# Kernel optimization log

Hardware: AMD Instinct MI355X
Metric: run time of the kernel (lower is better)

The kernel has to match this reference:

```python
import math
import jax, jax.numpy as jnp
import numpy as np

N_EXPERTS = 8
CAPACITY_FACTOR = 1.25
AUX_COEF = 0.01  # forward passes aux_loss_coef to BOTH z-loss and lb-loss


def setup_inputs() -> dict:
    key = jax.random.key(0)
    k1, k2 = jax.random.split(key)
    B, T, D = 4, 4096, 2048
    x = jax.random.normal(k1, (B, T, D), dtype=jnp.float32)
    # nn.Linear(d_model, n_experts, bias=False) weight: (n_experts, d_model)
    W = jax.random.normal(k2, (N_EXPERTS, D), dtype=jnp.float32) * (1.0 / math.sqrt(D))
    return {"x": x, "W": W}


def reference(x, W):
    B, T, D = x.shape
    S = B * T
    E = W.shape[0]
    capacity = int(math.ceil(S / E * CAPACITY_FACTOR))  # static

    x_flat = x.reshape(S, D)
    logits = jnp.einsum("sd,ed->se", x_flat, W)          # (S, E)
    probs = jax.nn.softmax(logits, axis=-1)               # (S, E)
    gate_vals = jnp.max(probs, axis=-1)                   # (S,)
    expert_idx = jnp.argmax(probs, axis=-1)               # (S,) int

    # rank of each token within its expert's queue (token order), 0-based
    onehot = jax.nn.one_hot(expert_idx, E, dtype=jnp.int32)        # (S, E)
    rank = jnp.sum(jnp.cumsum(onehot, axis=0) * onehot, axis=-1) - 1  # (S,)
    keep = rank < capacity
    kept_gates = jnp.where(keep, gate_vals, jnp.zeros((), gate_vals.dtype))

    # z-loss: coef * mean(logsumexp(logits)^2)
    log_z = jax.scipy.special.logsumexp(logits, axis=-1)
    z_loss = AUX_COEF * jnp.mean(log_z * log_z)

    # load-balance loss: coef * E * sum(f_i * p_i)
    p = jnp.mean(probs, axis=0)                                     # (E,)
    counts = jnp.zeros((E,), dtype=probs.dtype).at[expert_idx].add(1.0)
    f = counts / S
    lb_loss = AUX_COEF * E * jnp.sum(f * p)

    aux_loss = z_loss + lb_loss
    return expert_idx, kept_gates, aux_loss
```

## Files before the change

### kernel.cpp

```cpp
#include <hip/hip_runtime.h>

#define S_TOKENS 16384
#define DMODEL   2048
#define NE       8
#define CAPACITY 2560
#define AUXC     0.01f


__global__ void init_kernel(float* __restrict__ acc) {
    int t = threadIdx.x;
    if (t < 9) acc[t] = 0.0f;
}

__global__ __launch_bounds__(512, 1) void logits_kernel(
    const float* __restrict__ x, const float* __restrict__ W,
    int* __restrict__ idx_out, float* __restrict__ gate_out,
    float* __restrict__ psum, float* __restrict__ zsum) {
    __shared__ float4 WA[DMODEL];
    __shared__ float4 WB[DMODEL];

    const int tid  = threadIdx.x;
    const int wave = tid >> 6;
    const int lane = tid & 63;

    for (int j = tid; j < DMODEL; j += 512) {
        WA[j] = make_float4(W[j],          W[DMODEL + j],   W[2*DMODEL + j], W[3*DMODEL + j]);
        WB[j] = make_float4(W[4*DMODEL+j], W[5*DMODEL + j], W[6*DMODEL + j], W[7*DMODEL + j]);
    }
    __syncthreads();

    float pacc = 0.0f;
    float zacc = 0.0f;

    for (int gi = 0; gi < 4; ++gi) {
        const int group = blockIdx.x * 4 + gi;
        const int token = group * 8 + wave;
        const float* __restrict__ xrow = x + (size_t)token * DMODEL;

        float a0=0,a1=0,a2=0,a3=0,a4=0,a5=0,a6=0,a7=0;
        #pragma unroll 8
        for (int k = 0; k < DMODEL/64; ++k) {
            float  xv = xrow[k*64 + lane];
            float4 wa = WA[k*64 + lane];
            float4 wb = WB[k*64 + lane];
            a0 += xv*wa.x; a1 += xv*wa.y; a2 += xv*wa.z; a3 += xv*wa.w;
            a4 += xv*wb.x; a5 += xv*wb.y; a6 += xv*wb.z; a7 += xv*wb.w;
        }
        #pragma unroll
        for (int off = 32; off > 0; off >>= 1) {
            a0 += __shfl_xor(a0, off); a1 += __shfl_xor(a1, off);
            a2 += __shfl_xor(a2, off); a3 += __shfl_xor(a3, off);
            a4 += __shfl_xor(a4, off); a5 += __shfl_xor(a5, off);
            a6 += __shfl_xor(a6, off); a7 += __shfl_xor(a7, off);
        }
        float m = a0; int e = 0;
        if (a1 > m) { m = a1; e = 1; }
        if (a2 > m) { m = a2; e = 2; }
        if (a3 > m) { m = a3; e = 3; }
        if (a4 > m) { m = a4; e = 4; }
        if (a5 > m) { m = a5; e = 5; }
        if (a6 > m) { m = a6; e = 6; }
        if (a7 > m) { m = a7; e = 7; }
        float z = expf(a0-m)+expf(a1-m)+expf(a2-m)+expf(a3-m)
                + expf(a4-m)+expf(a5-m)+expf(a6-m)+expf(a7-m);
        float gate = 1.0f / z;
        float lz   = m + logf(z);

        if (lane == 0) {
            idx_out[token]  = e;
            gate_out[token] = gate;
            zacc += lz * lz;
        }
        float ae = a0;
        if (lane == 1) ae = a1;
        if (lane == 2) ae = a2;
        if (lane == 3) ae = a3;
        if (lane == 4) ae = a4;
        if (lane == 5) ae = a5;
        if (lane == 6) ae = a6;
        if (lane == 7) ae = a7;
        if (lane < NE) pacc += expf(ae - m) * gate;
    }

    __syncthreads();
    float* red = (float*)WA;
    float* zrd = (float*)WB;
    if (lane < NE)  red[wave*8 + lane] = pacc;
    if (lane == 0)  zrd[wave] = zacc;
    __syncthreads();
    if (tid < NE) {
        float s = 0.0f;
        #pragma unroll
        for (int w = 0; w < 8; ++w) s += red[w*8 + tid];
        atomicAdd(&psum[tid], s);
    }
    if (tid == NE) {
        float s = 0.0f;
        #pragma unroll
        for (int w = 0; w < 8; ++w) s += zrd[w];
        atomicAdd(zsum, s);
    }
}

__global__ __launch_bounds__(256, 1) void scan_kernel(
    const int* __restrict__ idx, int* __restrict__ prefix,
    const float* __restrict__ psum, const float* __restrict__ zsum,
    float* __restrict__ aux_out) {
    __shared__ int arr[NE][256];
    const int t = threadIdx.x;

    unsigned clo = 0, chi = 0;
    const int base = t * 64;
    #pragma unroll 8
    for (int i = 0; i < 64; ++i) {
        int e = idx[base + i];
        if (e < 4) clo += 1u << (8*e);
        else       chi += 1u << (8*(e-4));
    }
    int cnt[8];
    cnt[0] = clo & 255; cnt[1] = (clo >> 8) & 255; cnt[2] = (clo >> 16) & 255; cnt[3] = clo >> 24;
    cnt[4] = chi & 255; cnt[5] = (chi >> 8) & 255; cnt[6] = (chi >> 16) & 255; cnt[7] = chi >> 24;
    #pragma unroll
    for (int e = 0; e < NE; ++e) arr[e][t] = cnt[e];
    __syncthreads();

    for (int off = 1; off < 256; off <<= 1) {
        int v[8];
        #pragma unroll
        for (int e = 0; e < NE; ++e) v[e] = (t >= off) ? arr[e][t - off] : 0;
        __syncthreads();
        #pragma unroll
        for (int e = 0; e < NE; ++e) arr[e][t] += v[e];
        __syncthreads();
    }
    #pragma unroll
    for (int e = 0; e < NE; ++e) prefix[t*8 + e] = arr[e][t] - cnt[e];

    if (t == 0) {
        float lb = 0.0f;
        for (int e = 0; e < NE; ++e) {
            float f = (float)arr[e][255] / (float)S_TOKENS;
            float p = psum[e] / (float)S_TOKENS;
            lb += f * p;
        }
        lb *= AUXC * (float)NE;
        float zl = AUXC * (zsum[0] / (float)S_TOKENS);
        aux_out[0] = zl + lb;
    }
}

__global__ __launch_bounds__(64, 1) void output_kernel(
    const int* __restrict__ idx, const float* __restrict__ gate,
    const int* __restrict__ prefix, float* __restrict__ out) {
    const int b = blockIdx.x;
    const int l = threadIdx.x;
    const int token = b*64 + l;
    const int e = idx[token];

    unsigned long long mymask = 0;
    #pragma unroll
    for (int q = 0; q < NE; ++q) {
        unsigned long long msk = __ballot(e == q);
        if (e == q) mymask = msk;
    }
    unsigned long long lt = (1ull << l) - 1ull;
    int rank = prefix[b*8 + e] + __popcll(mymask & lt);

    out[token] = (float)e;
    out[S_TOKENS + token] = (rank < CAPACITY) ? gate[token] : 0.0f;
}

extern "C" void kernel_launch(void* const* d_in, const int* in_sizes, int n_in,
                              void* d_out, int out_size, void* d_ws, size_t ws_size,
                              hipStream_t stream) {
    const float* x = (const float*)d_in[0];
    const float* W = (const float*)d_in[1];
    float* out = (float*)d_out;

    int*   ws_idx    = (int*)d_ws;
    float* ws_gate   = (float*)d_ws + 16384;
    int*   ws_prefix = (int*)d_ws + 32768;
    float* ws_psum   = (float*)d_ws + 34816;
    float* ws_zsum   = (float*)d_ws + 34824;

    init_kernel<<<1, 64, 0, stream>>>(ws_psum);
    logits_kernel<<<512, 512, 0, stream>>>(x, W, ws_idx, ws_gate, ws_psum, ws_zsum);
    scan_kernel<<<1, 256, 0, stream>>>(ws_idx, ws_prefix, ws_psum, ws_zsum, out + 2*S_TOKENS);
    output_kernel<<<256, 64, 0, stream>>>(ws_idx, ws_gate, ws_prefix, out);
}
```

Measured before the change: 209.7 us.

## Register-block 4 tokens per wave with float4 loads and drop atomics/init kernel

```diff
diff --git a/kernel.cpp b/kernel.cpp
--- a/kernel.cpp
+++ b/kernel.cpp
@@ -7,115 +7,149 @@
 #define AUXC     0.01f
 
 
-__global__ void init_kernel(float* __restrict__ acc) {
-    int t = threadIdx.x;
-    if (t < 9) acc[t] = 0.0f;
-}
-
-__global__ __launch_bounds__(512, 1) void logits_kernel(
+__global__ __launch_bounds__(512, 4) void logits_kernel(
     const float* __restrict__ x, const float* __restrict__ W,
     int* __restrict__ idx_out, float* __restrict__ gate_out,
-    float* __restrict__ psum, float* __restrict__ zsum) {
-    __shared__ float4 WA[DMODEL];
-    __shared__ float4 WB[DMODEL];
+    float* __restrict__ bsums) {
+    __shared__ float4 WE[NE * 512];
 
     const int tid  = threadIdx.x;
     const int wave = tid >> 6;
     const int lane = tid & 63;
 
-    for (int j = tid; j < DMODEL; j += 512) {
-        WA[j] = make_float4(W[j],          W[DMODEL + j],   W[2*DMODEL + j], W[3*DMODEL + j]);
-        WB[j] = make_float4(W[4*DMODEL+j], W[5*DMODEL + j], W[6*DMODEL + j], W[7*DMODEL + j]);
-    }
-    __syncthreads();
+    {
+        const float4* __restrict__ Wf4 = (const float4*)W;
+        #pragma unroll
+        for (int i = 0; i < 8; ++i) WE[i * 512 + tid] = Wf4[i * 512 + tid];
+    }
+    __syncthreads();
+
+    const int t0 = blockIdx.x * 32 + wave * 4;
+    const float4* __restrict__ xr0 = (const float4*)x + (size_t)(t0 + 0) * (DMODEL / 4);
+    const float4* __restrict__ xr1 = (const float4*)x + (size_t)(t0 + 1) * (DMODEL / 4);
+    const float4* __restrict__ xr2 = (const float4*)x + (size_t)(t0 + 2) * (DMODEL / 4);
+    const float4* __restrict__ xr3 = (const float4*)x + (size_t)(t0 + 3) * (DMODEL / 4);
+
+    float acc[4][NE];
+    #pragma unroll
+    for (int t = 0; t < 4; ++t) {
+        #pragma unroll
+        for (int e = 0; e < NE; ++e) acc[t][e] = 0.0f;
+    }
+
+    #pragma unroll 2
+    for (int it = 0; it < (DMODEL / 4) / 64; ++it) {
+        const int j = it * 64 + lane;
+        float4 xv0 = xr0[j];
+        float4 xv1 = xr1[j];
+        float4 xv2 = xr2[j];
+        float4 xv3 = xr3[j];
+        #pragma unroll
+        for (int e = 0; e < NE; ++e) {
+            float4 w = WE[e * 512 + j];
+            acc[0][e] += xv0.x * w.x + xv0.y * w.y + xv0.z * w.z + xv0.w * w.w;
+            acc[1][e] += xv1.x * w.x + xv1.y * w.y + xv1.z * w.z + xv1.w * w.w;
+            acc[2][e] += xv2.x * w.x + xv2.y * w.y + xv2.z * w.z + xv2.w * w.w;
+            acc[3][e] += xv3.x * w.x + xv3.y * w.y + xv3.z * w.z + xv3.w * w.w;
+        }
+    }
+
+    const int  eL = lane >> 3;
+    const bool b5 = (lane & 32) != 0;
+    const bool b4 = (lane & 16) != 0;
+    const bool b3 = (lane & 8)  != 0;
 
     float pacc = 0.0f;
     float zacc = 0.0f;
 
-    for (int gi = 0; gi < 4; ++gi) {
-        const int group = blockIdx.x * 4 + gi;
-        const int token = group * 8 + wave;
-        const float* __restrict__ xrow = x + (size_t)token * DMODEL;
-
-        float a0=0,a1=0,a2=0,a3=0,a4=0,a5=0,a6=0,a7=0;
-        #pragma unroll 8
-        for (int k = 0; k < DMODEL/64; ++k) {
-            float  xv = xrow[k*64 + lane];
-            float4 wa = WA[k*64 + lane];
-            float4 wb = WB[k*64 + lane];
-            a0 += xv*wa.x; a1 += xv*wa.y; a2 += xv*wa.z; a3 += xv*wa.w;
-            a4 += xv*wb.x; a5 += xv*wb.y; a6 += xv*wb.z; a7 += xv*wb.w;
-        }
-        #pragma unroll
-        for (int off = 32; off > 0; off >>= 1) {
-            a0 += __shfl_xor(a0, off); a1 += __shfl_xor(a1, off);
-            a2 += __shfl_xor(a2, off); a3 += __shfl_xor(a3, off);
-            a4 += __shfl_xor(a4, off); a5 += __shfl_xor(a5, off);
-            a6 += __shfl_xor(a6, off); a7 += __shfl_xor(a7, off);
-        }
-        float m = a0; int e = 0;
-        if (a1 > m) { m = a1; e = 1; }
-        if (a2 > m) { m = a2; e = 2; }
-        if (a3 > m) { m = a3; e = 3; }
-        if (a4 > m) { m = a4; e = 4; }
-        if (a5 > m) { m = a5; e = 5; }
-        if (a6 > m) { m = a6; e = 6; }
-        if (a7 > m) { m = a7; e = 7; }
-        float z = expf(a0-m)+expf(a1-m)+expf(a2-m)+expf(a3-m)
-                + expf(a4-m)+expf(a5-m)+expf(a6-m)+expf(a7-m);
+    #pragma unroll
+    for (int t = 0; t < 4; ++t) {
+        float b[4];
+        #pragma unroll
+        for (int i = 0; i < 4; ++i) {
+            float keepv = b5 ? acc[t][i + 4] : acc[t][i];
+            float sendv = b5 ? acc[t][i]     : acc[t][i + 4];
+            b[i] = keepv + __shfl_xor(sendv, 32);
+        }
+        float c[2];
+        #pragma unroll
+        for (int i = 0; i < 2; ++i) {
+            float keepv = b4 ? b[i + 2] : b[i];
+            float sendv = b4 ? b[i]     : b[i + 2];
+            c[i] = keepv + __shfl_xor(sendv, 16);
+        }
+        float keepv = b3 ? c[1] : c[0];
+        float sendv = b3 ? c[0] : c[1];
+        float d = keepv + __shfl_xor(sendv, 8);
+        d += __shfl_xor(d, 1);
+        d += __shfl_xor(d, 2);
+        d += __shfl_xor(d, 4);
+
+        float m = d;
+        m = fmaxf(m, __shfl_xor(m, 8));
+        m = fmaxf(m, __shfl_xor(m, 16));
+        m = fmaxf(m, __shfl_xor(m, 32));
+        int cand = (d == m) ? eL : NE;
+        cand = min(cand, __shfl_xor(cand, 8));
+        cand = min(cand, __shfl_xor(cand, 16));
+        cand = min(cand, __shfl_xor(cand, 32));
+        float p = expf(d - m);
+        float z = p;
+        z += __shfl_xor(z, 8);
+        z += __shfl_xor(z, 16);
+        z += __shfl_xor(z, 32);
         float gate = 1.0f / z;
-        float lz   = m + logf(z);
-
+
+        if ((lane & 7) == 0) pacc += p * gate;
         if (lane == 0) {
-            idx_out[token]  = e;
+            const int token = t0 + t;
+            idx_out[token]  = cand;
             gate_out[token] = gate;
+            float lz = m + logf(z);
             zacc += lz * lz;
         }
-        float ae = a0;
-        if (lane == 1) ae = a1;
-        if (lane == 2) ae = a2;
-        if (lane == 3) ae = a3;
-        if (lane == 4) ae = a4;
-        if (lane == 5) ae = a5;
-        if (lane == 6) ae = a6;
-        if (lane == 7) ae = a7;
-        if (lane < NE) pacc += expf(ae - m) * gate;
-    }
-
-    __syncthreads();
-    float* red = (float*)WA;
-    float* zrd = (float*)WB;
-    if (lane < NE)  red[wave*8 + lane] = pacc;
-    if (lane == 0)  zrd[wave] = zacc;
+    }
+
+    __syncthreads();
+    float* red = (float*)WE;
+    float* zrd = (float*)WE + 64;
+    if ((lane & 7) == 0) red[wave * 8 + eL] = pacc;
+    if (lane == 0)       zrd[wave] = zacc;
     __syncthreads();
     if (tid < NE) {
         float s = 0.0f;
         #pragma unroll
-        for (int w = 0; w < 8; ++w) s += red[w*8 + tid];
-        atomicAdd(&psum[tid], s);
-    }
-    if (tid == NE) {
+        for (int w = 0; w < 8; ++w) s += red[w * 8 + tid];
+        bsums[blockIdx.x * 12 + tid] = s;
+    } else if (tid == NE) {
         float s = 0.0f;
         #pragma unroll
         for (int w = 0; w < 8; ++w) s += zrd[w];
-        atomicAdd(zsum, s);
+        bsums[blockIdx.x * 12 + NE] = s;
     }
 }
 
 __global__ __launch_bounds__(256, 1) void scan_kernel(
     const int* __restrict__ idx, int* __restrict__ prefix,
-    const float* __restrict__ psum, const float* __restrict__ zsum,
-    float* __restrict__ aux_out) {
-    __shared__ int arr[NE][256];
+    const float* __restrict__ bsums, float* __restrict__ aux_out) {
+    __shared__ int   arr[NE][256];
+    __shared__ float bs[9][256];
+    __shared__ float ptot[9];
     const int t = threadIdx.x;
 
+    #pragma unroll
+    for (int q = 0; q < 9; ++q)
+        bs[q][t] = bsums[t * 12 + q] + bsums[(t + 256) * 12 + q];
+
     unsigned clo = 0, chi = 0;
-    const int base = t * 64;
-    #pragma unroll 8
-    for (int i = 0; i < 64; ++i) {
-        int e = idx[base + i];
-        if (e < 4) clo += 1u << (8*e);
-        else       chi += 1u << (8*(e-4));
+    const int4* __restrict__ idx4 = (const int4*)idx;
+    #pragma unroll 4
+    for (int i = 0; i < 16; ++i) {
+        int4 v = idx4[t * 16 + i];
+        if (v.x < 4) clo += 1u << (8 * v.x); else chi += 1u << (8 * (v.x - 4));
+        if (v.y < 4) clo += 1u << (8 * v.y); else chi += 1u << (8 * (v.y - 4));
+        if (v.z < 4) clo += 1u << (8 * v.z); else chi += 1u << (8 * (v.z - 4));
+        if (v.w < 4) clo += 1u << (8 * v.w); else chi += 1u << (8 * (v.w - 4));
     }
     int cnt[8];
     cnt[0] = clo & 255; cnt[1] = (clo >> 8) & 255; cnt[2] = (clo >> 16) & 255; cnt[3] = clo >> 24;
@@ -124,6 +158,22 @@
     for (int e = 0; e < NE; ++e) arr[e][t] = cnt[e];
     __syncthreads();
 
+    if (t < 64) {
+        float s[9];
+        #pragma unroll
+        for (int q = 0; q < 9; ++q)
+            s[q] = bs[q][t] + bs[q][t + 64] + bs[q][t + 128] + bs[q][t + 192];
+        #pragma unroll
+        for (int off = 32; off > 0; off >>= 1) {
+            #pragma unroll
+            for (int q = 0; q < 9; ++q) s[q] += __shfl_xor(s[q], off);
+        }
+        if (t == 0) {
+            #pragma unroll
+            for (int q = 0; q < 9; ++q) ptot[q] = s[q];
+        }
+    }
+
     for (int off = 1; off < 256; off <<= 1) {
         int v[8];
         #pragma unroll
@@ -134,17 +184,18 @@
         __syncthreads();
     }
     #pragma unroll
-    for (int e = 0; e < NE; ++e) prefix[t*8 + e] = arr[e][t] - cnt[e];
+    for (int e = 0; e < NE; ++e) prefix[t * 8 + e] = arr[e][t] - cnt[e];
 
     if (t == 0) {
         float lb = 0.0f;
+        #pragma unroll
         for (int e = 0; e < NE; ++e) {
             float f = (float)arr[e][255] / (float)S_TOKENS;
-            float p = psum[e] / (float)S_TOKENS;
+            float p = ptot[e] / (float)S_TOKENS;
             lb += f * p;
         }
         lb *= AUXC * (float)NE;
-        float zl = AUXC * (zsum[0] / (float)S_TOKENS);
+        float zl = AUXC * (ptot[8] / (float)S_TOKENS);
         aux_out[0] = zl + lb;
     }
 }
@@ -154,7 +205,7 @@
     const int* __restrict__ prefix, float* __restrict__ out) {
     const int b = blockIdx.x;
     const int l = threadIdx.x;
-    const int token = b*64 + l;
+    const int token = b * 64 + l;
     const int e = idx[token];
 
     unsigned long long mymask = 0;
@@ -164,7 +215,7 @@
         if (e == q) mymask = msk;
     }
     unsigned long long lt = (1ull << l) - 1ull;
-    int rank = prefix[b*8 + e] + __popcll(mymask & lt);
+    int rank = prefix[b * 8 + e] + __popcll(mymask & lt);
 
     out[token] = (float)e;
     out[S_TOKENS + token] = (rank < CAPACITY) ? gate[token] : 0.0f;
@@ -180,11 +231,9 @@
     int*   ws_idx    = (int*)d_ws;
     float* ws_gate   = (float*)d_ws + 16384;
     int*   ws_prefix = (int*)d_ws + 32768;
-    float* ws_psum   = (float*)d_ws + 34816;
-    float* ws_zsum   = (float*)d_ws + 34824;
-
-    init_kernel<<<1, 64, 0, stream>>>(ws_psum);
-    logits_kernel<<<512, 512, 0, stream>>>(x, W, ws_idx, ws_gate, ws_psum, ws_zsum);
-    scan_kernel<<<1, 256, 0, stream>>>(ws_idx, ws_prefix, ws_psum, ws_zsum, out + 2*S_TOKENS);
+    float* ws_bsums  = (float*)d_ws + 34816;
+
+    logits_kernel<<<512, 512, 0, stream>>>(x, W, ws_idx, ws_gate, ws_bsums);
+    scan_kernel<<<1, 256, 0, stream>>>(ws_idx, ws_prefix, ws_bsums, out + 2 * S_TOKENS);
     output_kernel<<<256, 64, 0, stream>>>(ws_idx, ws_gate, ws_prefix, out);
 }
```

New measurement: 205.2 us. 1.02x faster.
